# Kernel tuning notes

Measured on AMD Instinct MI355X. Metric: run time of the kernel, lower is better.

Reference implementation:

```python
import jax, jax.numpy as jnp
import numpy as np

EPS = 1e-8
LAM = 0.7  # resonance_lambda


def phase_resonance(a, b, eps=EPS):
    # a, b: (B, N, D) float32. Pairwise phase coherence -> (B, N, N)
    D = a.shape[-1]
    pairs = (D // 2)
    a2 = a[..., :pairs * 2].reshape(*a.shape[:-1], pairs, 2)
    b2 = b[..., :pairs * 2].reshape(*b.shape[:-1], pairs, 2)
    theta_a = jnp.arctan2(a2[..., 1] + eps, a2[..., 0] + eps)  # (B,N,pairs)
    theta_b = jnp.arctan2(b2[..., 1] + eps, b2[..., 0] + eps)  # (B,N,pairs)
    delta = theta_a[:, :, None, :] - theta_b[:, None, :, :]    # (B,N,N,pairs)
    return jnp.cos(delta).mean(axis=-1)                        # (B,N,N)


def setup_inputs() -> dict:
    key = jax.random.key(0)
    k1, k2, k3, k4, k5 = jax.random.split(key, 5)
    B, N, D = 2, 1024, 128
    node_states = jax.random.normal(k1, (B, N, D), dtype=jnp.float32)
    node_gates = jax.random.uniform(k2, (B, N, 1), dtype=jnp.float32)
    r_acc = jax.random.normal(k3, (B, N, N), dtype=jnp.float32)
    # nn.Linear(D, D, bias=False) weights, y = x @ W.T
    scale = 1.0 / np.sqrt(D)
    W_in = jax.random.uniform(k4, (D, D), dtype=jnp.float32, minval=-scale, maxval=scale)
    W_out = jax.random.uniform(k5, (D, D), dtype=jnp.float32, minval=-scale, maxval=scale)
    conductance = jnp.asarray(1.0, dtype=jnp.float32)
    return {"node_states": node_states, "node_gates": node_gates, "r_acc": r_acc,
            "W_in": W_in, "W_out": W_out, "conductance": conductance}


def reference(node_states, node_gates, r_acc, W_in, W_out, conductance):
    B, N, D = node_states.shape
    h = node_states @ W_in.T                                   # field_in projection
    r_instant = phase_resonance(h, h)                          # (B,N,N)
    r_acc_new = LAM * r_acc + (1.0 - LAM) * r_instant
    r_acc_new = jnp.clip(r_acc_new, -2.0, 2.0)
    cond = jnp.clip(conductance, -5.0, 5.0)
    coupling = jax.nn.sigmoid(cond * r_acc_new)                # (B,N,N)
    eye = jnp.eye(N, dtype=coupling.dtype)[None]               # zero self-coupling
    coupling = coupling * (1.0 - eye)
    coupling = coupling * jnp.swapaxes(node_gates, -1, -2)     # (B,1,N) col gates
    coupling = coupling * node_gates                           # (B,N,1) row gates
    coupling = coupling / (coupling.sum(axis=-1, keepdims=True) + 1e-8)
    transmitted = node_states * node_gates
    values = transmitted @ W_out.T                             # field_out projection
    field_signal = coupling @ values                           # (B,N,D)
    return field_signal, r_acc_new
```

## Files before the change

kernel.cpp:

```cpp
#include <hip/hip_runtime.h>
#include <hip/hip_bf16.h>

using bf16x8 = __attribute__((ext_vector_type(8))) short;
using f32x4  = __attribute__((ext_vector_type(4))) float;

#define NN 1024
#define DD 128

__device__ __forceinline__ short bf16b(float f) {
    __hip_bfloat16 t = __float2bfloat16(f);
    return *(short*)&t;
}

__device__ __forceinline__ bf16x8 cvt8(const float* __restrict__ p) {
    float4 a = *(const float4*)p;
    float4 b = *(const float4*)(p + 4);
    bf16x8 r;
    r[0] = bf16b(a.x); r[1] = bf16b(a.y); r[2] = bf16b(a.z); r[3] = bf16b(a.w);
    r[4] = bf16b(b.x); r[5] = bf16b(b.y); r[6] = bf16b(b.z); r[7] = bf16b(b.w);
    return r;
}

__global__ __launch_bounds__(256) void prep_kernel(
    const float* __restrict__ states, const float* __restrict__ gates,
    const float* __restrict__ W_in, const float* __restrict__ W_out,
    __hip_bfloat16* __restrict__ M_bf, __hip_bfloat16* __restrict__ valT)
{
    __shared__ __align__(16) short s_m[16][136];
    __shared__ __align__(16) short s_vT[128][24];

    const int tid = threadIdx.x;
    const int l = tid & 63, w = tid >> 6;
    const int row_a = l & 15, kg = l >> 4;
    const int b  = blockIdx.x >> 6;
    const int n0 = (blockIdx.x & 63) * 16;
    const int colbase = w * 32;

    const float* A = states + ((size_t)b * NN + n0) * DD;

    f32x4 accH[2], accV[2];
    #pragma unroll
    for (int cp = 0; cp < 2; ++cp) {
        accH[cp] = (f32x4){0.f, 0.f, 0.f, 0.f};
        accV[cp] = (f32x4){0.f, 0.f, 0.f, 0.f};
    }

    #pragma unroll
    for (int ks = 0; ks < 4; ++ks) {
        int koff = (ks * 4 + kg) * 8;
        bf16x8 a = cvt8(A + row_a * DD + koff);
        #pragma unroll
        for (int cp = 0; cp < 2; ++cp) {
            int d = colbase + cp * 16 + row_a;
            bf16x8 b1 = cvt8(W_in  + d * DD + koff);
            bf16x8 b2 = cvt8(W_out + d * DD + koff);
            accH[cp] = __builtin_amdgcn_mfma_f32_16x16x32_bf16(a, b1, accH[cp], 0, 0, 0);
            accV[cp] = __builtin_amdgcn_mfma_f32_16x16x32_bf16(a, b2, accV[cp], 0, 0, 0);
        }
    }

    float g[4];
    #pragma unroll
    for (int q = 0; q < 4; ++q) g[q] = gates[b * NN + n0 + kg * 4 + q];

    const bool odd = (row_a & 1) != 0;
    #pragma unroll
    for (int cp = 0; cp < 2; ++cp) {
        #pragma unroll
        for (int q = 0; q < 4; ++q) {
            float hm = accH[cp][q] + 1e-8f;
            float hp = __shfl_xor(hm, 1);
            float x = odd ? hp : hm;
            float y = odd ? hm : hp;
            float r2 = x * x + y * y;
            float out;
            if (r2 > 0.f) out = (odd ? y : x) * rsqrtf(r2);
            else          out = odd ? 0.f : 1.f;
            s_m[kg * 4 + q][colbase + cp * 16 + row_a] = bf16b(out);
            s_vT[colbase + cp * 16 + row_a][kg * 4 + q] = bf16b(accV[cp][q] * g[q]);
        }
    }
    __syncthreads();

    {
        int r = tid >> 4, seg = tid & 15;
        bf16x8 v = *(const bf16x8*)&s_m[r][seg * 8];
        *(bf16x8*)(M_bf + ((size_t)b * NN + n0 + r) * DD + seg * 8) = v;
    }
    {
        int d = tid >> 1, half = tid & 1;
        bf16x8 v = *(const bf16x8*)&s_vT[d][half * 8];
        *(bf16x8*)(valT + ((size_t)b * DD + d) * NN + n0 + half * 8) = v;
    }
}

__global__ __launch_bounds__(256) void fused_kernel(
    const __hip_bfloat16* __restrict__ M_bf,
    const __hip_bfloat16* __restrict__ valT,
    const float* __restrict__ r_acc,
    const float* __restrict__ gates,
    const float* __restrict__ cond_ptr,
    float* __restrict__ r_out,
    __hip_bfloat16* __restrict__ part,
    float* __restrict__ part_rs)
{
    __shared__ __align__(16) short s_cpl[2][16][136];
    __shared__ float s_rs[32][2];

    const int tid = threadIdx.x;
    const int l  = tid & 63;
    const int w  = tid >> 6;
    const int wi = w & 1;
    const int wj = w >> 1;
    const int row_a = l & 15;
    const int kg    = l >> 4;

    const int jt = blockIdx.x;
    const int j0 = jt * 128;
    const int i0 = blockIdx.y * 32;
    const int b  = blockIdx.z;

    const bf16x8* Mv = (const bf16x8*)(M_bf + (size_t)b * NN * DD);
    const bf16x8* Vv = (const bf16x8*)(valT + (size_t)b * DD * NN);

    f32x4 acc[4];
    #pragma unroll
    for (int cp = 0; cp < 4; ++cp) acc[cp] = (f32x4){0.f, 0.f, 0.f, 0.f};

    #pragma unroll
    for (int ks = 0; ks < 4; ++ks) {
        int kv = ks * 4 + kg;
        bf16x8 a = Mv[(size_t)(i0 + wi * 16 + row_a) * 16 + kv];
        #pragma unroll
        for (int cp = 0; cp < 4; ++cp) {
            bf16x8 bb = Mv[(size_t)(j0 + wj * 64 + cp * 16 + row_a) * 16 + kv];
            acc[cp] = __builtin_amdgcn_mfma_f32_16x16x32_bf16(a, bb, acc[cp], 0, 0, 0);
        }
    }

    float cond = fminf(fmaxf(cond_ptr[0], -5.f), 5.f);
    const int i_base = i0 + wi * 16 + kg * 4;

    float g_j[4], g_i[4];
    #pragma unroll
    for (int cp = 0; cp < 4; ++cp) g_j[cp] = gates[b * NN + j0 + wj * 64 + cp * 16 + row_a];
    #pragma unroll
    for (int q = 0; q < 4; ++q)    g_i[q]  = gates[b * NN + i_base + q];

    const size_t robase = (size_t)b * NN * NN;
    float rs[4] = {0.f, 0.f, 0.f, 0.f};

    #pragma unroll
    for (int q = 0; q < 4; ++q) {
        int i = i_base + q;
        float gi = g_i[q];
        #pragma unroll
        for (int cp = 0; cp < 4; ++cp) {
            int jl = wj * 64 + cp * 16 + row_a;
            int j  = j0 + jl;
            float s  = acc[cp][q] * (1.f / 64.f);
            float ra = r_acc[robase + (size_t)i * NN + j];
            float rn = fminf(fmaxf(0.7f * ra + 0.3f * s, -2.f), 2.f);
            r_out[robase + (size_t)i * NN + j] = rn;
            float cpl = (i == j) ? 0.f
                        : (1.f / (1.f + __expf(-cond * rn))) * gi * g_j[cp];
            rs[q] += cpl;
            s_cpl[wi][kg * 4 + q][jl] = bf16b(cpl);
        }
    }

    #pragma unroll
    for (int q = 0; q < 4; ++q) {
        float v = rs[q];
        v += __shfl_xor(v, 1);
        v += __shfl_xor(v, 2);
        v += __shfl_xor(v, 4);
        v += __shfl_xor(v, 8);
        if (row_a == 0) s_rs[wi * 16 + kg * 4 + q][wj] = v;
    }
    __syncthreads();

    f32x4 pacc[4];
    #pragma unroll
    for (int dt = 0; dt < 4; ++dt) pacc[dt] = (f32x4){0.f, 0.f, 0.f, 0.f};

    #pragma unroll
    for (int ks2 = 0; ks2 < 4; ++ks2) {
        bf16x8 a = *(const bf16x8*)&s_cpl[wi][row_a][(ks2 * 4 + kg) * 8];
        #pragma unroll
        for (int dt = 0; dt < 4; ++dt) {
            int d = wj * 64 + dt * 16 + row_a;
            bf16x8 bb = Vv[(size_t)d * (NN / 8) + (j0 >> 3) + ks2 * 4 + kg];
            pacc[dt] = __builtin_amdgcn_mfma_f32_16x16x32_bf16(a, bb, pacc[dt], 0, 0, 0);
        }
    }

    __hip_bfloat16* pb = part + ((size_t)jt * 2 + b) * NN * DD;
    #pragma unroll
    for (int dt = 0; dt < 4; ++dt) {
        #pragma unroll
        for (int q = 0; q < 4; ++q) {
            int i = i0 + wi * 16 + kg * 4 + q;
            int d = wj * 64 + dt * 16 + row_a;
            pb[(size_t)i * DD + d] = __float2bfloat16(pacc[dt][q]);
        }
    }

    if (tid < 32)
        part_rs[((size_t)jt * 2 + b) * NN + i0 + tid] = s_rs[tid][0] + s_rs[tid][1];
}

__global__ __launch_bounds__(256) void reduce_kernel(
    const __hip_bfloat16* __restrict__ part,
    const float* __restrict__ part_rs,
    float* __restrict__ field)
{
    int t   = blockIdx.x * 256 + threadIdx.x;
    int b   = t >> 15;
    int rem = t & 32767;
    int i   = rem >> 5;
    int d4  = (rem & 31) * 4;
    size_t ibase = (size_t)i * DD + d4;

    float s0 = 0.f, s1 = 0.f, s2 = 0.f, s3 = 0.f, rsum = 0.f;
    #pragma unroll
    for (int jt = 0; jt < 8; ++jt) {
        size_t slab = ((size_t)jt * 2 + b);
        uint2 u = *(const uint2*)(part + slab * NN * DD + ibase);
        s0 += __uint_as_float(u.x << 16);
        s1 += __uint_as_float(u.x & 0xffff0000u);
        s2 += __uint_as_float(u.y << 16);
        s3 += __uint_as_float(u.y & 0xffff0000u);
        rsum += part_rs[slab * NN + i];
    }
    float inv = 1.0f / (rsum + 1e-8f);
    float4 o = {s0 * inv, s1 * inv, s2 * inv, s3 * inv};
    *(float4*)(field + ((size_t)b * NN + i) * DD + d4) = o;
}

extern "C" void kernel_launch(void* const* d_in, const int* in_sizes, int n_in,
                              void* d_out, int out_size, void* d_ws, size_t ws_size,
                              hipStream_t stream) {
    const float* states = (const float*)d_in[0];
    const float* gates  = (const float*)d_in[1];
    const float* r_acc  = (const float*)d_in[2];
    const float* W_in   = (const float*)d_in[3];
    const float* W_out  = (const float*)d_in[4];
    const float* cond   = (const float*)d_in[5];

    float* field = (float*)d_out;
    float* r_out = field + 2 * NN * DD;

    char* ws = (char*)d_ws;
    __hip_bfloat16* M_bf    = (__hip_bfloat16*)ws;
    __hip_bfloat16* valT    = (__hip_bfloat16*)(ws + (512 << 10));
    __hip_bfloat16* part    = (__hip_bfloat16*)(ws + (1 << 20));
    float*          part_rs = (float*)(ws + (5 << 20));

    hipLaunchKernelGGL(prep_kernel, dim3(128), dim3(256), 0, stream,
                       states, gates, W_in, W_out, M_bf, valT);
    hipLaunchKernelGGL(fused_kernel, dim3(8, 32, 2), dim3(256), 0, stream,
                       M_bf, valT, r_acc, gates, cond, r_out, part, part_rs);
    hipLaunchKernelGGL(reduce_kernel, dim3(256), dim3(256), 0, stream,
                       part, part_rs, field);
}
```

Before: 98.08 us.

## Fuse split-j reduction into main kernel by looping over column chunks per block

```diff
diff --git a/kernel.cpp b/kernel.cpp
--- a/kernel.cpp
+++ b/kernel.cpp
@@ -101,72 +101,87 @@
     const float* __restrict__ gates,
     const float* __restrict__ cond_ptr,
     float* __restrict__ r_out,
-    __hip_bfloat16* __restrict__ part,
-    float* __restrict__ part_rs)
+    float* __restrict__ field)
 {
-    __shared__ __align__(16) short s_cpl[2][16][136];
-    __shared__ float s_rs[32][2];
+    __shared__ __align__(16) short s_cpl[16][136];
+    __shared__ float s_rs[16][4];
+    __shared__ float s_gate[NN];
 
     const int tid = threadIdx.x;
-    const int l  = tid & 63;
-    const int w  = tid >> 6;
-    const int wi = w & 1;
-    const int wj = w >> 1;
-    const int row_a = l & 15;
-    const int kg    = l >> 4;
-
-    const int jt = blockIdx.x;
-    const int j0 = jt * 128;
-    const int i0 = blockIdx.y * 32;
-    const int b  = blockIdx.z;
+    const int l = tid & 63, w = tid >> 6;
+    const int row_a = l & 15, kg = l >> 4;
+    const int b  = blockIdx.x >> 6;
+    const int i0 = (blockIdx.x & 63) * 16;
 
     const bf16x8* Mv = (const bf16x8*)(M_bf + (size_t)b * NN * DD);
     const bf16x8* Vv = (const bf16x8*)(valT + (size_t)b * DD * NN);
 
-    f32x4 acc[4];
-    #pragma unroll
-    for (int cp = 0; cp < 4; ++cp) acc[cp] = (f32x4){0.f, 0.f, 0.f, 0.f};
-
-    #pragma unroll
-    for (int ks = 0; ks < 4; ++ks) {
-        int kv = ks * 4 + kg;
-        bf16x8 a = Mv[(size_t)(i0 + wi * 16 + row_a) * 16 + kv];
-        #pragma unroll
-        for (int cp = 0; cp < 4; ++cp) {
-            bf16x8 bb = Mv[(size_t)(j0 + wj * 64 + cp * 16 + row_a) * 16 + kv];
-            acc[cp] = __builtin_amdgcn_mfma_f32_16x16x32_bf16(a, bb, acc[cp], 0, 0, 0);
-        }
-    }
-
-    float cond = fminf(fmaxf(cond_ptr[0], -5.f), 5.f);
-    const int i_base = i0 + wi * 16 + kg * 4;
-
-    float g_j[4], g_i[4];
-    #pragma unroll
-    for (int cp = 0; cp < 4; ++cp) g_j[cp] = gates[b * NN + j0 + wj * 64 + cp * 16 + row_a];
-    #pragma unroll
-    for (int q = 0; q < 4; ++q)    g_i[q]  = gates[b * NN + i_base + q];
+    ((float4*)s_gate)[tid] = ((const float4*)(gates + (size_t)b * NN))[tid];
+
+    bf16x8 aF[4];
+    #pragma unroll
+    for (int ks = 0; ks < 4; ++ks)
+        aF[ks] = Mv[(size_t)(i0 + row_a) * 16 + ks * 4 + kg];
+
+    const float cond = fminf(fmaxf(cond_ptr[0], -5.f), 5.f);
+    float g_i[4];
+    #pragma unroll
+    for (int q = 0; q < 4; ++q) g_i[q] = gates[(size_t)b * NN + i0 + kg * 4 + q];
 
     const size_t robase = (size_t)b * NN * NN;
     float rs[4] = {0.f, 0.f, 0.f, 0.f};
-
-    #pragma unroll
-    for (int q = 0; q < 4; ++q) {
-        int i = i_base + q;
-        float gi = g_i[q];
-        #pragma unroll
-        for (int cp = 0; cp < 4; ++cp) {
-            int jl = wj * 64 + cp * 16 + row_a;
-            int j  = j0 + jl;
-            float s  = acc[cp][q] * (1.f / 64.f);
-            float ra = r_acc[robase + (size_t)i * NN + j];
-            float rn = fminf(fmaxf(0.7f * ra + 0.3f * s, -2.f), 2.f);
-            r_out[robase + (size_t)i * NN + j] = rn;
-            float cpl = (i == j) ? 0.f
-                        : (1.f / (1.f + __expf(-cond * rn))) * gi * g_j[cp];
-            rs[q] += cpl;
-            s_cpl[wi][kg * 4 + q][jl] = bf16b(cpl);
-        }
+    f32x4 pacc[2];
+    pacc[0] = (f32x4){0.f, 0.f, 0.f, 0.f};
+    pacc[1] = (f32x4){0.f, 0.f, 0.f, 0.f};
+
+    __syncthreads();
+
+    for (int jc = 0; jc < 8; ++jc) {
+        const int j0 = jc * 128;
+
+        f32x4 acc[2];
+        acc[0] = (f32x4){0.f, 0.f, 0.f, 0.f};
+        acc[1] = (f32x4){0.f, 0.f, 0.f, 0.f};
+        #pragma unroll
+        for (int ks = 0; ks < 4; ++ks) {
+            #pragma unroll
+            for (int cp = 0; cp < 2; ++cp) {
+                bf16x8 bb = Mv[(size_t)(j0 + w * 32 + cp * 16 + row_a) * 16 + ks * 4 + kg];
+                acc[cp] = __builtin_amdgcn_mfma_f32_16x16x32_bf16(aF[ks], bb, acc[cp], 0, 0, 0);
+            }
+        }
+
+        #pragma unroll
+        for (int q = 0; q < 4; ++q) {
+            const int i = i0 + kg * 4 + q;
+            const float gi = g_i[q];
+            #pragma unroll
+            for (int cp = 0; cp < 2; ++cp) {
+                const int jl = w * 32 + cp * 16 + row_a;
+                const int j  = j0 + jl;
+                float s  = acc[cp][q] * (1.f / 64.f);
+                float ra = r_acc[robase + (size_t)i * NN + j];
+                float rn = fminf(fmaxf(0.7f * ra + 0.3f * s, -2.f), 2.f);
+                r_out[robase + (size_t)i * NN + j] = rn;
+                float cpl = (i == j) ? 0.f
+                            : (1.f / (1.f + __expf(-cond * rn))) * gi * s_gate[j];
+                rs[q] += cpl;
+                s_cpl[kg * 4 + q][jl] = bf16b(cpl);
+            }
+        }
+        __syncthreads();
+
+        #pragma unroll
+        for (int ks2 = 0; ks2 < 4; ++ks2) {
+            bf16x8 a = *(const bf16x8*)&s_cpl[row_a][(ks2 * 4 + kg) * 8];
+            #pragma unroll
+            for (int dt = 0; dt < 2; ++dt) {
+                int d = w * 32 + dt * 16 + row_a;
+                bf16x8 bb = Vv[(size_t)d * (NN / 8) + jc * 16 + ks2 * 4 + kg];
+                pacc[dt] = __builtin_amdgcn_mfma_f32_16x16x32_bf16(a, bb, pacc[dt], 0, 0, 0);
+            }
+        }
+        __syncthreads();
     }
 
     #pragma unroll
@@ -176,66 +191,22 @@
         v += __shfl_xor(v, 2);
         v += __shfl_xor(v, 4);
         v += __shfl_xor(v, 8);
-        if (row_a == 0) s_rs[wi * 16 + kg * 4 + q][wj] = v;
+        if (row_a == 0) s_rs[kg * 4 + q][w] = v;
     }
     __syncthreads();
 
-    f32x4 pacc[4];
-    #pragma unroll
-    for (int dt = 0; dt < 4; ++dt) pacc[dt] = (f32x4){0.f, 0.f, 0.f, 0.f};
-
-    #pragma unroll
-    for (int ks2 = 0; ks2 < 4; ++ks2) {
-        bf16x8 a = *(const bf16x8*)&s_cpl[wi][row_a][(ks2 * 4 + kg) * 8];
-        #pragma unroll
-        for (int dt = 0; dt < 4; ++dt) {
-            int d = wj * 64 + dt * 16 + row_a;
-            bf16x8 bb = Vv[(size_t)d * (NN / 8) + (j0 >> 3) + ks2 * 4 + kg];
-            pacc[dt] = __builtin_amdgcn_mfma_f32_16x16x32_bf16(a, bb, pacc[dt], 0, 0, 0);
-        }
-    }
-
-    __hip_bfloat16* pb = part + ((size_t)jt * 2 + b) * NN * DD;
-    #pragma unroll
-    for (int dt = 0; dt < 4; ++dt) {
-        #pragma unroll
-        for (int q = 0; q < 4; ++q) {
-            int i = i0 + wi * 16 + kg * 4 + q;
-            int d = wj * 64 + dt * 16 + row_a;
-            pb[(size_t)i * DD + d] = __float2bfloat16(pacc[dt][q]);
-        }
-    }
-
-    if (tid < 32)
-        part_rs[((size_t)jt * 2 + b) * NN + i0 + tid] = s_rs[tid][0] + s_rs[tid][1];
-}
-
-__global__ __launch_bounds__(256) void reduce_kernel(
-    const __hip_bfloat16* __restrict__ part,
-    const float* __restrict__ part_rs,
-    float* __restrict__ field)
-{
-    int t   = blockIdx.x * 256 + threadIdx.x;
-    int b   = t >> 15;
-    int rem = t & 32767;
-    int i   = rem >> 5;
-    int d4  = (rem & 31) * 4;
-    size_t ibase = (size_t)i * DD + d4;
-
-    float s0 = 0.f, s1 = 0.f, s2 = 0.f, s3 = 0.f, rsum = 0.f;
-    #pragma unroll
-    for (int jt = 0; jt < 8; ++jt) {
-        size_t slab = ((size_t)jt * 2 + b);
-        uint2 u = *(const uint2*)(part + slab * NN * DD + ibase);
-        s0 += __uint_as_float(u.x << 16);
-        s1 += __uint_as_float(u.x & 0xffff0000u);
-        s2 += __uint_as_float(u.y << 16);
-        s3 += __uint_as_float(u.y & 0xffff0000u);
-        rsum += part_rs[slab * NN + i];
-    }
-    float inv = 1.0f / (rsum + 1e-8f);
-    float4 o = {s0 * inv, s1 * inv, s2 * inv, s3 * inv};
-    *(float4*)(field + ((size_t)b * NN + i) * DD + d4) = o;
+    #pragma unroll
+    for (int q = 0; q < 4; ++q) {
+        const int i = i0 + kg * 4 + q;
+        float rsum = s_rs[kg * 4 + q][0] + s_rs[kg * 4 + q][1]
+                   + s_rs[kg * 4 + q][2] + s_rs[kg * 4 + q][3];
+        float inv = 1.0f / (rsum + 1e-8f);
+        #pragma unroll
+        for (int dt = 0; dt < 2; ++dt) {
+            int d = w * 32 + dt * 16 + row_a;
+            field[((size_t)b * NN + i) * DD + d] = pacc[dt][q] * inv;
+        }
+    }
 }
 
 extern "C" void kernel_launch(void* const* d_in, const int* in_sizes, int n_in,
@@ -252,15 +223,11 @@
     float* r_out = field + 2 * NN * DD;
 
     char* ws = (char*)d_ws;
-    __hip_bfloat16* M_bf    = (__hip_bfloat16*)ws;
-    __hip_bfloat16* valT    = (__hip_bfloat16*)(ws + (512 << 10));
-    __hip_bfloat16* part    = (__hip_bfloat16*)(ws + (1 << 20));
-    float*          part_rs = (float*)(ws + (5 << 20));
+    __hip_bfloat16* M_bf = (__hip_bfloat16*)ws;
+    __hip_bfloat16* valT = (__hip_bfloat16*)(ws + (512 << 10));
 
     hipLaunchKernelGGL(prep_kernel, dim3(128), dim3(256), 0, stream,
                        states, gates, W_in, W_out, M_bf, valT);
-    hipLaunchKernelGGL(fused_kernel, dim3(8, 32, 2), dim3(256), 0, stream,
-                       M_bf, valT, r_acc, gates, cond, r_out, part, part_rs);
-    hipLaunchKernelGGL(reduce_kernel, dim3(256), dim3(256), 0, stream,
-                       part, part_rs, field);
-}
+    hipLaunchKernelGGL(fused_kernel, dim3(128), dim3(256), 0, stream,
+                       M_bf, valT, r_acc, gates, cond, r_out, field);
+}
```

New measurement: 119.0 us. 21.3% more time.
